# Kernel tuning notes

Measured on AMD Instinct MI355X. Metric: run time of the kernel, lower is better.

The kernel has to match this reference:

```python
import jax, jax.numpy as jnp
import numpy as np

TOP_K = 2


def setup_inputs() -> dict:
    key = jax.random.key(0)
    ks = jax.random.split(key, 6)
    B, S, H, I, E = 2, 1024, 1024, 2048, 8
    s_h = 1.0 / np.sqrt(H)
    s_i = 1.0 / np.sqrt(I)
    return {
        "x": jax.random.normal(ks[0], (B, S, H), jnp.float32),
        "gate_w": jax.random.normal(ks[1], (H, E), jnp.float32) * s_h,
        "gate_b": jnp.zeros((E,), jnp.float32),
        "w1": jax.random.normal(ks[2], (E, H, I), jnp.float32) * s_h,
        "w3": jax.random.normal(ks[3], (E, H, I), jnp.float32) * s_h,
        "w2": jax.random.normal(ks[4], (E, I, H), jnp.float32) * s_i,
    }


def reference(x, gate_w, gate_b, w1, w3, w2):
    # Gating: softmax over experts, then top-k selection + renormalization.
    logits = jnp.einsum("bsh,he->bse", x, gate_w) + gate_b            # [B,S,E]
    probs = jax.nn.softmax(logits, axis=-1)
    topk_w, topk_idx = jax.lax.top_k(probs, TOP_K)                    # [B,S,K]
    topk_w = topk_w / jnp.sum(topk_w, axis=-1, keepdims=True)

    E = gate_w.shape[-1]
    # Per-token combine weight for each expert (0 if not routed there).
    # one_hot: [B,S,K,E] -> combine: [B,S,E]
    combine = jnp.sum(jax.nn.one_hot(topk_idx, E, dtype=x.dtype) * topk_w[..., None], axis=-2)

    # SwiGLU expert FFN: down(silu(gate(x)) * up(x)); dense-masked reference
    # (compute every expert on every token, weight by combine; math identical
    # to the original gather/scatter loop since combine is 0 off-route).
    out = jnp.zeros_like(x)
    for e in range(E):
        h = jax.nn.silu(x @ w1[e]) * (x @ w3[e])                      # [B,S,I]
        out = out + combine[..., e:e + 1] * (h @ w2[e])               # [B,S,H]
    return out
```

## Files before the change

### kernel.cpp

```cpp
#include <hip/hip_runtime.h>
#include <hip/hip_bf16.h>
#include <math.h>

typedef __attribute__((ext_vector_type(4))) float f32x4;
typedef __attribute__((ext_vector_type(8))) short bf16x8;

#define T_TOK 2048
#define H_DIM 1024
#define I_DIM 2048
#define E_NUM 8

__device__ inline unsigned short f2bf(float f) {
  union { float f; unsigned int u; } v; v.f = f;
  unsigned int r = v.u + 0x7fffu + ((v.u >> 16) & 1u);
  return (unsigned short)(r >> 16);
}
__device__ inline unsigned int pack2(float a, float b) {
  return (unsigned int)f2bf(a) | ((unsigned int)f2bf(b) << 16);
}

__device__ inline void gld16(const void* g, void* l) {
  __builtin_amdgcn_global_load_lds((const __attribute__((address_space(1))) void*)g,
                                   (__attribute__((address_space(3))) void*)l, 16, 0, 0);
}

__device__ inline void transpose_pair(const float* __restrict__ ip, unsigned short* __restrict__ op,
                                      int R, int C, int rp, int ct, char* smem)
{
  unsigned short (*tl)[66] = (unsigned short (*)[66])smem;
  int r0 = rp * 128, c0 = ct * 64;
  int tid = threadIdx.x;
  int rq = (tid >> 4) * 4;
  int c4 = (tid & 15) * 4;
  const float* b0 = ip + (size_t)(r0 + rq) * C + c0 + c4;
  const float* b1 = b0 + (size_t)64 * C;
  float4 v[8];
  v[0] = *(const float4*)(b0);
  v[1] = *(const float4*)(b0 + C);
  v[2] = *(const float4*)(b0 + 2 * C);
  v[3] = *(const float4*)(b0 + 3 * C);
  v[4] = *(const float4*)(b1);
  v[5] = *(const float4*)(b1 + C);
  v[6] = *(const float4*)(b1 + 2 * C);
  v[7] = *(const float4*)(b1 + 3 * C);
  const float* f = (const float*)v;
#pragma unroll
  for (int j = 0; j < 4; ++j) {
    *(unsigned int*)&tl[c4 + j][rq]          = pack2(f[0 * 4 + j], f[1 * 4 + j]);
    *(unsigned int*)&tl[c4 + j][rq + 2]      = pack2(f[2 * 4 + j], f[3 * 4 + j]);
    *(unsigned int*)&tl[64 + c4 + j][rq]     = pack2(f[4 * 4 + j], f[5 * 4 + j]);
    *(unsigned int*)&tl[64 + c4 + j][rq + 2] = pack2(f[6 * 4 + j], f[7 * 4 + j]);
  }
  __syncthreads();
  int c = tid >> 3, r8 = (tid & 7) * 8;
#pragma unroll
  for (int it = 0; it < 2; ++it) {
    int cc = c + it * 32;
#pragma unroll
    for (int p = 0; p < 2; ++p) {
      uint4 o;
      o.x = *(const unsigned int*)&tl[p * 64 + cc][r8];
      o.y = *(const unsigned int*)&tl[p * 64 + cc][r8 + 2];
      o.z = *(const unsigned int*)&tl[p * 64 + cc][r8 + 4];
      o.w = *(const unsigned int*)&tl[p * 64 + cc][r8 + 6];
      *(uint4*)(op + (size_t)(c0 + cc) * R + r0 + p * 64 + r8) = o;
    }
  }
}

__global__ __launch_bounds__(256) void gate_t13(
    const float* __restrict__ x, const float* __restrict__ gw, const float* __restrict__ gb,
    int* __restrict__ rec_e, float* __restrict__ rec_w, unsigned short* __restrict__ xb,
    const float* __restrict__ w1, const float* __restrict__ w3,
    unsigned short* __restrict__ w1t, unsigned short* __restrict__ w3t)
{
  __shared__ __align__(16) char smem[128 * 66 * 2];
  int bx = blockIdx.x;
  if (bx >= 512) {
    int idx = bx - 512;
    int m = idx >> 8;
    int t8 = idx & 255;
    int rp = t8 & 7;
    int ct = t8 >> 3;
    const float* ip = (m < 8 ? w1 : w3) + (size_t)(m & 7) * ((size_t)H_DIM * I_DIM);
    unsigned short* op = (m < 8 ? w1t : w3t) + (size_t)(m & 7) * ((size_t)H_DIM * I_DIM);
    transpose_pair(ip, op, H_DIM, I_DIM, rp, ct, smem);
    return;
  }
  int wv = threadIdx.x >> 6, lane = threadIdx.x & 63;
  int t = bx * 4 + wv;
  const float* xr = x + (size_t)t * H_DIM;
  unsigned short* xo = xb + (size_t)t * H_DIM;
  float acc[8];
#pragma unroll
  for (int e = 0; e < 8; ++e) acc[e] = 0.f;
  for (int i = 0; i < H_DIM / 64; ++i) {
    int h = i * 64 + lane;
    float xv = xr[h];
    xo[h] = f2bf(xv);
    const float4* g = (const float4*)(gw + (size_t)h * 8);
    float4 g0 = g[0], g1 = g[1];
    acc[0] += xv * g0.x; acc[1] += xv * g0.y; acc[2] += xv * g0.z; acc[3] += xv * g0.w;
    acc[4] += xv * g1.x; acc[5] += xv * g1.y; acc[6] += xv * g1.z; acc[7] += xv * g1.w;
  }
#pragma unroll
  for (int s = 1; s < 64; s <<= 1) {
#pragma unroll
    for (int e = 0; e < 8; ++e) acc[e] += __shfl_xor(acc[e], s);
  }
  if (lane == 0) {
    float l[8];
#pragma unroll
    for (int e = 0; e < 8; ++e) l[e] = acc[e] + gb[e];
    int e0 = 0;
    for (int e = 1; e < 8; ++e) if (l[e] > l[e0]) e0 = e;
    int e1 = (e0 == 0) ? 1 : 0;
    for (int e = 0; e < 8; ++e) if (e != e0 && l[e] > l[e1]) e1 = e;
    float w0 = 1.f / (1.f + expf(l[e1] - l[e0]));
    rec_e[t * 2]     = e0; rec_e[t * 2 + 1] = e1;
    rec_w[t * 2]     = w0; rec_w[t * 2 + 1] = 1.f - w0;
  }
}

__global__ __launch_bounds__(256) void route8(
    const int* __restrict__ rec_e, const float* __restrict__ rec_w,
    int* __restrict__ counts_g, int* __restrict__ list_tok, float* __restrict__ list_w)
{
  __shared__ int cnt[8];
  __shared__ int fill;
  int e = blockIdx.x;
  int tid = threadIdx.x;
  if (tid < 8) cnt[tid] = 0;
  if (tid == 0) fill = 0;
  __syncthreads();
  int e_loc[16];
  int c_loc[8];
#pragma unroll
  for (int k = 0; k < 8; ++k) c_loc[k] = 0;
#pragma unroll
  for (int it = 0; it < 16; ++it) {
    e_loc[it] = rec_e[it * 256 + tid] & 7;
    c_loc[e_loc[it]]++;
  }
#pragma unroll
  for (int k = 0; k < 8; ++k) if (c_loc[k]) atomicAdd(&cnt[k], c_loc[k]);
  __syncthreads();
  if (e == 0 && tid < 8) counts_g[tid] = cnt[tid];
  int base = 0;
#pragma unroll
  for (int k = 0; k < 8; ++k) if (k < e) base += cnt[k];
#pragma unroll
  for (int it = 0; it < 16; ++it) {
    if (e_loc[it] == e) {
      int i = it * 256 + tid;
      int pos = atomicAdd(&fill, 1);
      list_tok[base + pos] = i;
      list_w[base + pos]   = rec_w[i];
    }
  }
}

__global__ __launch_bounds__(256, 2) void gemm1_t2(
    const unsigned short* __restrict__ xb,
    const unsigned short* __restrict__ w1t,
    const unsigned short* __restrict__ w3t,
    const int* __restrict__ counts,
    const int* __restrict__ list_tok,
    unsigned short* __restrict__ hbuf,
    const float* __restrict__ w2,
    unsigned short* __restrict__ w2t)
{
  __shared__ __align__(16) char smem[49152];
  int bx = blockIdx.x;
  if (bx >= 4096) {
    int idx = bx - 4096;
    int e = idx >> 8;
    int t8 = idx & 255;
    int rp = t8 & 15;
    int ct = t8 >> 4;
    const float* ip = w2 + (size_t)e * ((size_t)H_DIM * I_DIM);
    unsigned short* op = w2t + (size_t)e * ((size_t)H_DIM * I_DIM);
    transpose_pair(ip, op, I_DIM, H_DIM, rp, ct, smem);
    return;
  }
  int e = bx >> 9;
  int y = (bx >> 4) & 31;
  int ix = bx & 15;
  int nbase = 0;
#pragma unroll
  for (int i = 0; i < 8; ++i) if (i < e) nbase += counts[i];
  int n_e = counts[e];
  int t0 = y * 128;
  if (t0 >= n_e) return;
  int i0 = ix * 128;

  char* As  = smem;
  char* B1s = smem + 16384;
  char* B3s = smem + 32768;

  int tid = threadIdx.x;
  int r2 = tid >> 2;
  int seg = (tid & 3) * 8;

  int sr0 = t0 + r2;       if (sr0 >= n_e) sr0 = n_e - 1;
  int sr1 = t0 + 64 + r2;  if (sr1 >= n_e) sr1 = n_e - 1;
  int tok0 = list_tok[nbase + sr0] >> 1;
  int tok1 = list_tok[nbase + sr1] >> 1;
  const char* gA0 = (const char*)(xb + (size_t)tok0 * H_DIM + seg);
  const char* gA1 = (const char*)(xb + (size_t)tok1 * H_DIM + seg);
  const char* gB1a = (const char*)(w1t + ((size_t)e * I_DIM + i0 + r2) * H_DIM + seg);
  const char* gB1b = (const char*)(w1t + ((size_t)e * I_DIM + i0 + 64 + r2) * H_DIM + seg);
  const char* gB3a = (const char*)(w3t + ((size_t)e * I_DIM + i0 + r2) * H_DIM + seg);
  const char* gB3b = (const char*)(w3t + ((size_t)e * I_DIM + i0 + 64 + r2) * H_DIM + seg);

  int w = tid >> 6, lane = tid & 63, lm = lane & 15, lq = lane >> 4;
  int wm = w & 1, wn = w >> 1;

  f32x4 acc1[4][4], acc3[4][4];
#pragma unroll
  for (int i = 0; i < 4; ++i)
#pragma unroll
    for (int j = 0; j < 4; ++j) { acc1[i][j] = (f32x4){0,0,0,0}; acc3[i][j] = (f32x4){0,0,0,0}; }

  for (int kb = 0; kb < H_DIM; kb += 64) {
    __syncthreads();
    gld16(gA0 + kb * 2,       As + tid * 16);
    gld16(gA1 + kb * 2,       As + 4096 + tid * 16);
    gld16(gA0 + kb * 2 + 64,  As + 8192 + tid * 16);
    gld16(gA1 + kb * 2 + 64,  As + 12288 + tid * 16);
    gld16(gB1a + kb * 2,      B1s + tid * 16);
    gld16(gB1b + kb * 2,      B1s + 4096 + tid * 16);
    gld16(gB1a + kb * 2 + 64, B1s + 8192 + tid * 16);
    gld16(gB1b + kb * 2 + 64, B1s + 12288 + tid * 16);
    gld16(gB3a + kb * 2,      B3s + tid * 16);
    gld16(gB3b + kb * 2,      B3s + 4096 + tid * 16);
    gld16(gB3a + kb * 2 + 64, B3s + 8192 + tid * 16);
    gld16(gB3b + kb * 2 + 64, B3s + 12288 + tid * 16);
    __syncthreads();
#pragma unroll
    for (int s = 0; s < 2; ++s) {
      bf16x8 a[4], b1[4], b3[4];
#pragma unroll
      for (int i = 0; i < 4; ++i)
        a[i] = *(const bf16x8*)(As + s * 8192 + ((wm * 64 + i * 16 + lm) * 32 + lq * 8) * 2);
#pragma unroll
      for (int j = 0; j < 4; ++j) {
        b1[j] = *(const bf16x8*)(B1s + s * 8192 + ((wn * 64 + j * 16 + lm) * 32 + lq * 8) * 2);
        b3[j] = *(const bf16x8*)(B3s + s * 8192 + ((wn * 64 + j * 16 + lm) * 32 + lq * 8) * 2);
      }
#pragma unroll
      for (int i = 0; i < 4; ++i)
#pragma unroll
        for (int j = 0; j < 4; ++j) {
          acc1[i][j] = __builtin_amdgcn_mfma_f32_16x16x32_bf16(a[i], b1[j], acc1[i][j], 0, 0, 0);
          acc3[i][j] = __builtin_amdgcn_mfma_f32_16x16x32_bf16(a[i], b3[j], acc3[i][j], 0, 0, 0);
        }
    }
  }

#pragma unroll
  for (int i = 0; i < 4; ++i) {
#pragma unroll
    for (int rr = 0; rr < 4; ++rr) {
      int slot = t0 + wm * 64 + i * 16 + lq * 4 + rr;
      if (slot < n_e) {
        unsigned short* orow = hbuf + (size_t)(nbase + slot) * I_DIM + i0 + wn * 64 + lm;
#pragma unroll
        for (int j = 0; j < 4; ++j) {
          float g = acc1[i][j][rr], u = acc3[i][j][rr];
          float hv = (g / (1.f + __expf(-g))) * u;
          orow[j * 16] = f2bf(hv);
        }
      }
    }
  }
}

__global__ __launch_bounds__(256, 4) void gemm2(
    const unsigned short* __restrict__ hbuf,
    const unsigned short* __restrict__ w2t,
    const int* __restrict__ counts,
    const int* __restrict__ list_tok,
    const float* __restrict__ list_w,
    float* __restrict__ partial)
{
  __shared__ __align__(16) char smem[24576];
  int e = blockIdx.z;
  int nbase = 0;
#pragma unroll
  for (int i = 0; i < 8; ++i) if (i < e) nbase += counts[i];
  int n_e = counts[e];
  int ts = blockIdx.y >> 1, kh = blockIdx.y & 1;
  int t0 = ts * 64;
  if (t0 >= n_e) return;
  int h0 = blockIdx.x * 128;
  int k0 = kh * (I_DIM / 2);

  char* As = smem;
  char* Bs = smem + 8192;

  int tid = threadIdx.x;
  int r2 = tid >> 2;
  int seg = (tid & 3) * 8;

  int sr = t0 + r2; if (sr >= n_e) sr = n_e - 1;
  const char* gA  = (const char*)(hbuf + (size_t)(nbase + sr) * I_DIM + k0 + seg);
  const char* gB0 = (const char*)(w2t + ((size_t)e * H_DIM + h0 + r2) * I_DIM + k0 + seg);
  const char* gB1 = (const char*)(w2t + ((size_t)e * H_DIM + h0 + 64 + r2) * I_DIM + k0 + seg);

  int w = tid >> 6, lane = tid & 63, lm = lane & 15, lq = lane >> 4;
  int wm = w & 1, wn = (w >> 1) * 64;

  f32x4 acc[2][4];
#pragma unroll
  for (int i = 0; i < 2; ++i)
#pragma unroll
    for (int j = 0; j < 4; ++j) acc[i][j] = (f32x4){0,0,0,0};

  for (int kb = 0; kb < I_DIM / 2; kb += 64) {
    __syncthreads();
    gld16(gA + kb * 2,       As + tid * 16);
    gld16(gA + kb * 2 + 64,  As + 4096 + tid * 16);
    gld16(gB0 + kb * 2,      Bs + tid * 16);
    gld16(gB1 + kb * 2,      Bs + 4096 + tid * 16);
    gld16(gB0 + kb * 2 + 64, Bs + 8192 + tid * 16);
    gld16(gB1 + kb * 2 + 64, Bs + 12288 + tid * 16);
    __syncthreads();
#pragma unroll
    for (int s = 0; s < 2; ++s) {
      bf16x8 a[2], b[4];
#pragma unroll
      for (int i = 0; i < 2; ++i)
        a[i] = *(const bf16x8*)(As + s * 4096 + ((wm * 32 + i * 16 + lm) * 32 + lq * 8) * 2);
#pragma unroll
      for (int j = 0; j < 4; ++j)
        b[j] = *(const bf16x8*)(Bs + s * 8192 + ((wn + j * 16 + lm) * 32 + lq * 8) * 2);
#pragma unroll
      for (int i = 0; i < 2; ++i)
#pragma unroll
        for (int j = 0; j < 4; ++j)
          acc[i][j] = __builtin_amdgcn_mfma_f32_16x16x32_bf16(a[i], b[j], acc[i][j], 0, 0, 0);
    }
  }

  int entv[2][4]; float wtv[2][4];
#pragma unroll
  for (int i = 0; i < 2; ++i)
#pragma unroll
    for (int rr = 0; rr < 4; ++rr) {
      int slot = t0 + wm * 32 + i * 16 + lq * 4 + rr;
      if (slot < n_e) { entv[i][rr] = list_tok[nbase + slot]; wtv[i][rr] = list_w[nbase + slot]; }
      else entv[i][rr] = -1;
    }
#pragma unroll
  for (int i = 0; i < 2; ++i)
#pragma unroll
    for (int j = 0; j < 4; ++j)
#pragma unroll
      for (int rr = 0; rr < 4; ++rr) {
        if (entv[i][rr] >= 0) {
          int t = entv[i][rr] >> 1, kk = entv[i][rr] & 1;
          int plane = kh * 2 + kk;
          partial[((size_t)plane * T_TOK + t) * H_DIM + h0 + wn + j * 16 + lm] =
              acc[i][j][rr] * wtv[i][rr];
        }
      }
}

__global__ __launch_bounds__(256) void combine4(const float* __restrict__ partial,
                                                float* __restrict__ out)
{
  const size_t P = (size_t)T_TOK * H_DIM;
  size_t i = (size_t)(blockIdx.x * 256 + threadIdx.x) * 4;
  float4 a = *(const float4*)(partial + i);
  float4 b = *(const float4*)(partial + P + i);
  float4 c = *(const float4*)(partial + 2 * P + i);
  float4 d = *(const float4*)(partial + 3 * P + i);
  float4 o;
  o.x = a.x + b.x + c.x + d.x;
  o.y = a.y + b.y + c.y + d.y;
  o.z = a.z + b.z + c.z + d.z;
  o.w = a.w + b.w + c.w + d.w;
  *(float4*)(out + i) = o;
}

extern "C" void kernel_launch(void* const* d_in, const int* in_sizes, int n_in,
                              void* d_out, int out_size, void* d_ws, size_t ws_size,
                              hipStream_t stream) {
  const float* x  = (const float*)d_in[0];
  const float* gw = (const float*)d_in[1];
  const float* gb = (const float*)d_in[2];
  const float* w1 = (const float*)d_in[3];
  const float* w3 = (const float*)d_in[4];
  const float* w2 = (const float*)d_in[5];
  float* out = (float*)d_out;

  char* ws = (char*)d_ws;
  int*   counts   = (int*)(ws);
  int*   rec_e    = (int*)(ws + 128);
  float* rec_w    = (float*)(ws + 16512);
  int*   list_tok = (int*)(ws + 32896);
  float* list_w   = (float*)(ws + 49280);
  const size_t MB = 1024ull * 1024ull;
  unsigned short* xb   = (unsigned short*)(ws + 1 * MB);
  unsigned short* w1t  = (unsigned short*)(ws + 5 * MB);
  float* partial       = (float*)(ws + 5 * MB);
  unsigned short* w3t  = (unsigned short*)(ws + 37 * MB);
  unsigned short* w2t  = (unsigned short*)(ws + 69 * MB);
  unsigned short* hbuf = (unsigned short*)(ws + 101 * MB);

  gate_t13<<<512 + 4096, 256, 0, stream>>>(x, gw, gb, rec_e, rec_w, xb, w1, w3, w1t, w3t);
  route8<<<8, 256, 0, stream>>>(rec_e, rec_w, counts, list_tok, list_w);
  gemm1_t2<<<4096 + 2048, 256, 0, stream>>>(xb, w1t, w3t, counts, list_tok, hbuf, w2, w2t);
  gemm2<<<dim3(H_DIM / 128, 64, E_NUM), 256, 0, stream>>>(hbuf, w2t, counts, list_tok, list_w, partial);
  combine4<<<(T_TOK * H_DIM) / (256 * 4), 256, 0, stream>>>(partial, out);
}
```

Before: 333.2 us.

## Double-buffer LDS in both expert GEMMs with XOR swizzle and larger gemm2 tile

Both grouped GEMMs now use a two-stage LDS ping-pong with a 32-wide K step. The next tile's async global-to-LDS loads are issued before the MFMAs on the current tile, so each iteration needs one barrier instead of two. An XOR swizzle of the 16-byte segments by row is meant to reduce LDS bank conflicts on the fragment reads. gemm2's token tile grows from 64 to 128 rows with a 4x4 accumulator and occupancy 2, which raises reuse of the w2 tile at the cost of more registers and fewer resident blocks.

```diff
diff --git a/kernel.cpp b/kernel.cpp
--- a/kernel.cpp
+++ b/kernel.cpp
@@ -194,27 +194,35 @@
   if (t0 >= n_e) return;
   int i0 = ix * 128;
 
-  char* As  = smem;
-  char* B1s = smem + 16384;
-  char* B3s = smem + 32768;
-
   int tid = threadIdx.x;
   int r2 = tid >> 2;
-  int seg = (tid & 3) * 8;
+  int sseg = (((tid & 3) ^ (r2 & 3)) * 8);
 
   int sr0 = t0 + r2;       if (sr0 >= n_e) sr0 = n_e - 1;
   int sr1 = t0 + 64 + r2;  if (sr1 >= n_e) sr1 = n_e - 1;
   int tok0 = list_tok[nbase + sr0] >> 1;
   int tok1 = list_tok[nbase + sr1] >> 1;
-  const char* gA0 = (const char*)(xb + (size_t)tok0 * H_DIM + seg);
-  const char* gA1 = (const char*)(xb + (size_t)tok1 * H_DIM + seg);
-  const char* gB1a = (const char*)(w1t + ((size_t)e * I_DIM + i0 + r2) * H_DIM + seg);
-  const char* gB1b = (const char*)(w1t + ((size_t)e * I_DIM + i0 + 64 + r2) * H_DIM + seg);
-  const char* gB3a = (const char*)(w3t + ((size_t)e * I_DIM + i0 + r2) * H_DIM + seg);
-  const char* gB3b = (const char*)(w3t + ((size_t)e * I_DIM + i0 + 64 + r2) * H_DIM + seg);
+  const char* gA0  = (const char*)(xb + (size_t)tok0 * H_DIM + sseg);
+  const char* gA1  = (const char*)(xb + (size_t)tok1 * H_DIM + sseg);
+  const char* gB1a = (const char*)(w1t + ((size_t)e * I_DIM + i0 + r2) * H_DIM + sseg);
+  const char* gB1b = (const char*)(w1t + ((size_t)e * I_DIM + i0 + 64 + r2) * H_DIM + sseg);
+  const char* gB3a = (const char*)(w3t + ((size_t)e * I_DIM + i0 + r2) * H_DIM + sseg);
+  const char* gB3b = (const char*)(w3t + ((size_t)e * I_DIM + i0 + 64 + r2) * H_DIM + sseg);
+
+#define STAGE1(buf, kb) do {                              \
+    gld16(gA0  + (kb) * 2, (buf) + tid * 16);             \
+    gld16(gA1  + (kb) * 2, (buf) + 4096  + tid * 16);     \
+    gld16(gB1a + (kb) * 2, (buf) + 8192  + tid * 16);     \
+    gld16(gB1b + (kb) * 2, (buf) + 12288 + tid * 16);     \
+    gld16(gB3a + (kb) * 2, (buf) + 16384 + tid * 16);     \
+    gld16(gB3b + (kb) * 2, (buf) + 20480 + tid * 16);     \
+  } while (0)
 
   int w = tid >> 6, lane = tid & 63, lm = lane & 15, lq = lane >> 4;
   int wm = w & 1, wn = w >> 1;
+  int colx = (lq ^ (lm & 3)) * 16;
+  int rA = (wm * 64 + lm) * 64 + colx;
+  int rB = (wn * 64 + lm) * 64 + colx;
 
   f32x4 acc1[4][4], acc3[4][4];
 #pragma unroll
@@ -222,41 +230,31 @@
 #pragma unroll
     for (int j = 0; j < 4; ++j) { acc1[i][j] = (f32x4){0,0,0,0}; acc3[i][j] = (f32x4){0,0,0,0}; }
 
-  for (int kb = 0; kb < H_DIM; kb += 64) {
+  STAGE1(smem, 0);
+  __syncthreads();
+  for (int kb = 0; kb < H_DIM; kb += 32) {
+    char* cur = smem + (((kb >> 5) & 1) ? 24576 : 0);
+    char* nxt = smem + (((kb >> 5) & 1) ? 0 : 24576);
+    if (kb + 32 < H_DIM) STAGE1(nxt, kb + 32);
+    bf16x8 a[4], b1[4], b3[4];
+#pragma unroll
+    for (int i = 0; i < 4; ++i)
+      a[i] = *(const bf16x8*)(cur + rA + i * 1024);
+#pragma unroll
+    for (int j = 0; j < 4; ++j) {
+      b1[j] = *(const bf16x8*)(cur + 8192  + rB + j * 1024);
+      b3[j] = *(const bf16x8*)(cur + 16384 + rB + j * 1024);
+    }
+#pragma unroll
+    for (int i = 0; i < 4; ++i)
+#pragma unroll
+      for (int j = 0; j < 4; ++j) {
+        acc1[i][j] = __builtin_amdgcn_mfma_f32_16x16x32_bf16(a[i], b1[j], acc1[i][j], 0, 0, 0);
+        acc3[i][j] = __builtin_amdgcn_mfma_f32_16x16x32_bf16(a[i], b3[j], acc3[i][j], 0, 0, 0);
+      }
     __syncthreads();
-    gld16(gA0 + kb * 2,       As + tid * 16);
-    gld16(gA1 + kb * 2,       As + 4096 + tid * 16);
-    gld16(gA0 + kb * 2 + 64,  As + 8192 + tid * 16);
-    gld16(gA1 + kb * 2 + 64,  As + 12288 + tid * 16);
-    gld16(gB1a + kb * 2,      B1s + tid * 16);
-    gld16(gB1b + kb * 2,      B1s + 4096 + tid * 16);
-    gld16(gB1a + kb * 2 + 64, B1s + 8192 + tid * 16);
-    gld16(gB1b + kb * 2 + 64, B1s + 12288 + tid * 16);
-    gld16(gB3a + kb * 2,      B3s + tid * 16);
-    gld16(gB3b + kb * 2,      B3s + 4096 + tid * 16);
-    gld16(gB3a + kb * 2 + 64, B3s + 8192 + tid * 16);
-    gld16(gB3b + kb * 2 + 64, B3s + 12288 + tid * 16);
-    __syncthreads();
-#pragma unroll
-    for (int s = 0; s < 2; ++s) {
-      bf16x8 a[4], b1[4], b3[4];
-#pragma unroll
-      for (int i = 0; i < 4; ++i)
-        a[i] = *(const bf16x8*)(As + s * 8192 + ((wm * 64 + i * 16 + lm) * 32 + lq * 8) * 2);
-#pragma unroll
-      for (int j = 0; j < 4; ++j) {
-        b1[j] = *(const bf16x8*)(B1s + s * 8192 + ((wn * 64 + j * 16 + lm) * 32 + lq * 8) * 2);
-        b3[j] = *(const bf16x8*)(B3s + s * 8192 + ((wn * 64 + j * 16 + lm) * 32 + lq * 8) * 2);
-      }
-#pragma unroll
-      for (int i = 0; i < 4; ++i)
-#pragma unroll
-        for (int j = 0; j < 4; ++j) {
-          acc1[i][j] = __builtin_amdgcn_mfma_f32_16x16x32_bf16(a[i], b1[j], acc1[i][j], 0, 0, 0);
-          acc3[i][j] = __builtin_amdgcn_mfma_f32_16x16x32_bf16(a[i], b3[j], acc3[i][j], 0, 0, 0);
-        }
-    }
-  }
+  }
+#undef STAGE1
 
 #pragma unroll
   for (int i = 0; i < 4; ++i) {
@@ -276,7 +274,7 @@
   }
 }
 
-__global__ __launch_bounds__(256, 4) void gemm2(
+__global__ __launch_bounds__(256, 2) void gemm2(
     const unsigned short* __restrict__ hbuf,
     const unsigned short* __restrict__ w2t,
     const int* __restrict__ counts,
@@ -284,76 +282,81 @@
     const float* __restrict__ list_w,
     float* __restrict__ partial)
 {
-  __shared__ __align__(16) char smem[24576];
+  __shared__ __align__(16) char smem[32768];
   int e = blockIdx.z;
   int nbase = 0;
 #pragma unroll
   for (int i = 0; i < 8; ++i) if (i < e) nbase += counts[i];
   int n_e = counts[e];
   int ts = blockIdx.y >> 1, kh = blockIdx.y & 1;
-  int t0 = ts * 64;
+  int t0 = ts * 128;
   if (t0 >= n_e) return;
   int h0 = blockIdx.x * 128;
   int k0 = kh * (I_DIM / 2);
 
-  char* As = smem;
-  char* Bs = smem + 8192;
-
   int tid = threadIdx.x;
   int r2 = tid >> 2;
-  int seg = (tid & 3) * 8;
-
-  int sr = t0 + r2; if (sr >= n_e) sr = n_e - 1;
-  const char* gA  = (const char*)(hbuf + (size_t)(nbase + sr) * I_DIM + k0 + seg);
-  const char* gB0 = (const char*)(w2t + ((size_t)e * H_DIM + h0 + r2) * I_DIM + k0 + seg);
-  const char* gB1 = (const char*)(w2t + ((size_t)e * H_DIM + h0 + 64 + r2) * I_DIM + k0 + seg);
+  int sseg = (((tid & 3) ^ (r2 & 3)) * 8);
+
+  int sr0 = t0 + r2;       if (sr0 >= n_e) sr0 = n_e - 1;
+  int sr1 = t0 + 64 + r2;  if (sr1 >= n_e) sr1 = n_e - 1;
+  const char* gA0 = (const char*)(hbuf + (size_t)(nbase + sr0) * I_DIM + k0 + sseg);
+  const char* gA1 = (const char*)(hbuf + (size_t)(nbase + sr1) * I_DIM + k0 + sseg);
+  const char* gB0 = (const char*)(w2t + ((size_t)e * H_DIM + h0 + r2) * I_DIM + k0 + sseg);
+  const char* gB1 = (const char*)(w2t + ((size_t)e * H_DIM + h0 + 64 + r2) * I_DIM + k0 + sseg);
+
+#define STAGE2(buf, kb) do {                              \
+    gld16(gA0 + (kb) * 2, (buf) + tid * 16);              \
+    gld16(gA1 + (kb) * 2, (buf) + 4096  + tid * 16);      \
+    gld16(gB0 + (kb) * 2, (buf) + 8192  + tid * 16);      \
+    gld16(gB1 + (kb) * 2, (buf) + 12288 + tid * 16);      \
+  } while (0)
 
   int w = tid >> 6, lane = tid & 63, lm = lane & 15, lq = lane >> 4;
-  int wm = w & 1, wn = (w >> 1) * 64;
-
-  f32x4 acc[2][4];
-#pragma unroll
-  for (int i = 0; i < 2; ++i)
+  int wm = w & 1, wn = w >> 1;
+  int colx = (lq ^ (lm & 3)) * 16;
+  int rA = (wm * 64 + lm) * 64 + colx;
+  int rB = (wn * 64 + lm) * 64 + colx;
+
+  f32x4 acc[4][4];
+#pragma unroll
+  for (int i = 0; i < 4; ++i)
 #pragma unroll
     for (int j = 0; j < 4; ++j) acc[i][j] = (f32x4){0,0,0,0};
 
-  for (int kb = 0; kb < I_DIM / 2; kb += 64) {
+  STAGE2(smem, 0);
+  __syncthreads();
+  for (int kb = 0; kb < I_DIM / 2; kb += 32) {
+    char* cur = smem + (((kb >> 5) & 1) ? 16384 : 0);
+    char* nxt = smem + (((kb >> 5) & 1) ? 0 : 16384);
+    if (kb + 32 < I_DIM / 2) STAGE2(nxt, kb + 32);
+    bf16x8 a[4], b[4];
+#pragma unroll
+    for (int i = 0; i < 4; ++i)
+      a[i] = *(const bf16x8*)(cur + rA + i * 1024);
+#pragma unroll
+    for (int j = 0; j < 4; ++j)
+      b[j] = *(const bf16x8*)(cur + 8192 + rB + j * 1024);
+#pragma unroll
+    for (int i = 0; i < 4; ++i)
+#pragma unroll
+      for (int j = 0; j < 4; ++j)
+        acc[i][j] = __builtin_amdgcn_mfma_f32_16x16x32_bf16(a[i], b[j], acc[i][j], 0, 0, 0);
     __syncthreads();
-    gld16(gA + kb * 2,       As + tid * 16);
-    gld16(gA + kb * 2 + 64,  As + 4096 + tid * 16);
-    gld16(gB0 + kb * 2,      Bs + tid * 16);
-    gld16(gB1 + kb * 2,      Bs + 4096 + tid * 16);
-    gld16(gB0 + kb * 2 + 64, Bs + 8192 + tid * 16);
-    gld16(gB1 + kb * 2 + 64, Bs + 12288 + tid * 16);
-    __syncthreads();
-#pragma unroll
-    for (int s = 0; s < 2; ++s) {
-      bf16x8 a[2], b[4];
-#pragma unroll
-      for (int i = 0; i < 2; ++i)
-        a[i] = *(const bf16x8*)(As + s * 4096 + ((wm * 32 + i * 16 + lm) * 32 + lq * 8) * 2);
-#pragma unroll
-      for (int j = 0; j < 4; ++j)
-        b[j] = *(const bf16x8*)(Bs + s * 8192 + ((wn + j * 16 + lm) * 32 + lq * 8) * 2);
-#pragma unroll
-      for (int i = 0; i < 2; ++i)
-#pragma unroll
-        for (int j = 0; j < 4; ++j)
-          acc[i][j] = __builtin_amdgcn_mfma_f32_16x16x32_bf16(a[i], b[j], acc[i][j], 0, 0, 0);
-    }
-  }
-
-  int entv[2][4]; float wtv[2][4];
-#pragma unroll
-  for (int i = 0; i < 2; ++i)
+  }
+#undef STAGE2
+
+  int entv[4][4]; float wtv[4][4];
+#pragma unroll
+  for (int i = 0; i < 4; ++i)
 #pragma unroll
     for (int rr = 0; rr < 4; ++rr) {
-      int slot = t0 + wm * 32 + i * 16 + lq * 4 + rr;
+      int slot = t0 + wm * 64 + i * 16 + lq * 4 + rr;
       if (slot < n_e) { entv[i][rr] = list_tok[nbase + slot]; wtv[i][rr] = list_w[nbase + slot]; }
       else entv[i][rr] = -1;
     }
 #pragma unroll
-  for (int i = 0; i < 2; ++i)
+  for (int i = 0; i < 4; ++i)
 #pragma unroll
     for (int j = 0; j < 4; ++j)
 #pragma unroll
@@ -361,7 +364,7 @@
         if (entv[i][rr] >= 0) {
           int t = entv[i][rr] >> 1, kk = entv[i][rr] & 1;
           int plane = kh * 2 + kk;
-          partial[((size_t)plane * T_TOK + t) * H_DIM + h0 + wn + j * 16 + lm] =
+          partial[((size_t)plane * T_TOK + t) * H_DIM + h0 + wn * 64 + j * 16 + lm] =
               acc[i][j][rr] * wtv[i][rr];
         }
       }
```

Measured after the change: 344.2 us. 3.3% more time.
